# Kernel tuning notes

Measured on AMD Instinct MI355X. Metric: run time of the kernel, lower is better.

The kernel has to match this reference:

```python
import jax, jax.numpy as jnp
import numpy as np
import math

B, P = 64, 2048
E_DRUG, E_PATH = 512, 512
ATTN_DIM, H, DEPTH = 1024, 8, 1
HD = ATTN_DIM // (2 * H)          # head_dim = 64
SCALING = HD ** (-0.5)
LAMBDA_INIT = 0.8 - 0.6 * math.exp(-0.3 * DEPTH)
EPS_SM = 1e-20
EPS_RMS = 1e-5


def stable_softmax(x, eps=EPS_SM):
    x = x.astype(jnp.float32)
    x = x - jnp.max(x, axis=-1, keepdims=True)
    ex = jnp.exp(x)
    return ex / (jnp.sum(ex, axis=-1, keepdims=True) + eps)


def setup_inputs() -> dict:
    key = jax.random.key(0)
    ks = jax.random.split(key, 11)
    d = 2 * H * HD  # = ATTN_DIM
    return {
        "query": jax.random.normal(ks[0], (B, 1, E_DRUG), jnp.float32),
        "key": jax.random.normal(ks[1], (B, P, E_PATH), jnp.float32),
        # Linear weights stored [in, out] (transpose of torch storage; same math)
        "Wq": jax.random.normal(ks[2], (E_DRUG, d), jnp.float32) * 0.02,
        "Wk": jax.random.normal(ks[3], (E_PATH, d), jnp.float32) * 0.02,
        "Wv": jax.random.normal(ks[4], (E_PATH, d), jnp.float32) * 0.02,
        "Wo": jax.random.normal(ks[5], (d, E_DRUG), jnp.float32) * 0.02,
        "lambda_q1": jax.random.normal(ks[6], (HD,), jnp.float32) * 0.1,
        "lambda_k1": jax.random.normal(ks[7], (HD,), jnp.float32) * 0.1,
        "lambda_q2": jax.random.normal(ks[8], (HD,), jnp.float32) * 0.1,
        "lambda_k2": jax.random.normal(ks[9], (HD,), jnp.float32) * 0.1,
        "rms_weight": jnp.ones((2 * HD,), jnp.float32),
    }


def reference(query, key, Wq, Wk, Wv, Wo,
              lambda_q1, lambda_k1, lambda_q2, lambda_k2, rms_weight):
    # Q: [B,1,H,2,HD] -> [B,H,2,1,HD]; K,V: [B,P,H,2,HD] -> [B,H,2,P,HD]
    Q = (query @ Wq).reshape(B, 1, H, 2, HD).transpose(0, 2, 3, 1, 4) * SCALING
    K = (key @ Wk).reshape(B, P, H, 2, HD).transpose(0, 2, 3, 1, 4)
    V = (key @ Wv).reshape(B, P, H, 2, HD)

    # scores: [B,H,2,1,P]
    scores = jnp.einsum('bhsqd,bhskd->bhsqk', Q, K)
    scores = stable_softmax(scores)

    lam1 = jnp.exp(jnp.sum(lambda_q1 * lambda_k1))
    lam2 = jnp.exp(jnp.sum(lambda_q2 * lambda_k2))
    lam = lam1 - lam2 + LAMBDA_INIT

    diff_attn = scores[:, :, 0] - lam * scores[:, :, 1]  # [B,H,1,P]

    V_cat = V.transpose(0, 2, 1, 3, 4).reshape(B, H, P, 2 * HD)  # [B,H,P,2HD]
    out = jnp.einsum('bhqp,bhpd->bhqd', diff_attn, V_cat)        # [B,H,1,2HD]

    # RMSNorm over last dim, affine
    var = jnp.mean(out * out, axis=-1, keepdims=True)
    out = out * jax.lax.rsqrt(var + EPS_RMS) * rms_weight
    out = out * (1.0 - LAMBDA_INIT)

    out = out.transpose(0, 2, 1, 3).reshape(B, 1, 2 * H * HD)
    out = out @ Wo  # [B,1,E_DRUG]
    return out, diff_attn
```

## Files before the change

### kernel.cpp

```cpp
#include <hip/hip_runtime.h>
#include <hip/hip_bf16.h>
#include <math.h>

#define B_ 64
#define P_ 2048
#define E_ 512
#define H_ 8
#define D_ 1024
#define NC_ 32
#define NG_ 4
#define SMEM_FUSED (65536 + 8704 + 2304 + 64 + 64)

#define BAR() do { asm volatile("s_waitcnt lgkmcnt(0)" ::: "memory"); \
                   __builtin_amdgcn_s_barrier(); } while (0)

static constexpr float SCALING_C = 0.125f;
static constexpr float LAMBDA_INIT_C = 0.35550906759096966f;

typedef float f32x4 __attribute__((ext_vector_type(4)));
typedef float f32x2 __attribute__((ext_vector_type(2)));
typedef short bf16x8 __attribute__((ext_vector_type(8)));
typedef short bf16x4 __attribute__((ext_vector_type(4)));

static __device__ __forceinline__ short f2bf(float f) {
    unsigned u = __builtin_bit_cast(unsigned, f);
    unsigned r = (u + 0x7fffu + ((u >> 16) & 1u)) >> 16;
    return (short)r;
}

__global__ __launch_bounds__(256) void k_qproj(const float* __restrict__ query,
                                               const float* __restrict__ Wq,
                                               const float* __restrict__ Wk,
                                               unsigned short* __restrict__ qkfrag) {
    int x = blockIdx.x, b = blockIdx.y, t = threadIdx.x;
    __shared__ float q[E_];
    __shared__ float qh[256];
    q[t] = query[b * E_ + t];
    q[t + 256] = query[b * E_ + t + 256];
    __syncthreads();
    {
        int j = x * 256 + t;
        const float* w = Wq + j;
        float s[8] = {0.f,0.f,0.f,0.f,0.f,0.f,0.f,0.f};
        #pragma unroll 4
        for (int e = 0; e < E_; e += 8) {
            #pragma unroll
            for (int k = 0; k < 8; ++k) s[k] += q[e + k] * w[(long)(e + k) * D_];
        }
        qh[t] = (((s[0]+s[1])+(s[2]+s[3])) + ((s[4]+s[5])+(s[6]+s[7]))) * SCALING_C;
    }
    __syncthreads();
    int hs_loc = t >> 6, l = t & 63;
    int hs = x * 4 + hs_loc;
    int e0 = l * 8;
    const float* qp = qh + hs_loc * 64;
    float acc[8];
    #pragma unroll
    for (int jj = 0; jj < 8; ++jj) {
        const f32x4* w = (const f32x4*)(Wk + (long)(e0 + jj) * D_ + hs * 64);
        float s = 0.f;
        #pragma unroll
        for (int d4 = 0; d4 < 16; ++d4) {
            f32x4 wv = w[d4];
            s += qp[d4 * 4 + 0] * wv[0] + qp[d4 * 4 + 1] * wv[1]
               + qp[d4 * 4 + 2] * wv[2] + qp[d4 * 4 + 3] * wv[3];
        }
        acc[jj] = s;
    }
    bf16x8 v;
    #pragma unroll
    for (int jj = 0; jj < 8; ++jj) v[jj] = f2bf(acc[jj]);
    *(bf16x8*)(qkfrag + (((long)b * 16 + (l >> 2)) * 64 + (l & 3) * 16 + hs) * 8) = v;
}

__global__ __launch_bounds__(512, 2) void k_fusedp(const float* __restrict__ key,
                                                   const unsigned short* __restrict__ qkfrag,
                                                   float* __restrict__ wexp,
                                                   float* __restrict__ ms, float* __restrict__ zs,
                                                   float* __restrict__ apart) {
    extern __shared__ __align__(16) char smem[];
    unsigned short* kswz = (unsigned short*)smem;
    float* scr           = (float*)(smem + 65536);
    unsigned short* wbf  = (unsigned short*)(smem + 74240);
    float* fac_l         = (float*)(smem + 76544);
    float* mrun_l        = (float*)(smem + 76608);

    int pcg = blockIdx.x, b = blockIdx.y;
    int t = threadIdx.x, wv = t >> 6, l = t & 63;
    int rt = wv >> 1, eh = wv & 1;
    int prow = rt * 16 + (l & 15);
    int xorv = ((prow & 7) << 3) ^ ((prow & 8) << 1);
    int hi = t >> 7;
    int col4 = t & 127;

    if (t < 16) mrun_l[t] = -3.0e38f;

    bf16x8 qfr[8];
    {
        const bf16x8* qf = (const bf16x8*)(qkfrag + (long)b * 16 * 64 * 8);
        #pragma unroll
        for (int s = 0; s < 8; ++s) qfr[s] = qf[(eh * 8 + s) * 64 + l];
    }

    const float* kchunk = key + ((long)b * P_ + pcg * 512) * E_;

    f32x4 x[16];
    #pragma unroll
    for (int r = 0; r < 16; ++r)
        x[r] = *(const f32x4*)(kchunk + (long)(r * 512 + t) * 4);

    f32x4 accp[4];
    #pragma unroll
    for (int i = 0; i < 4; ++i) accp[i] = {0.f, 0.f, 0.f, 0.f};

    for (int c = 0; c < 8; ++c) {
        #pragma unroll
        for (int r = 0; r < 16; ++r) {
            int row = 4 * r + hi;
            int xr = ((row & 7) << 3) ^ ((row & 8) << 1);
            bf16x4 wb;
            wb[0] = f2bf(x[r][0]); wb[1] = f2bf(x[r][1]);
            wb[2] = f2bf(x[r][2]); wb[3] = f2bf(x[r][3]);
            *(bf16x4*)(kswz + row * 512 + ((col4 * 4) ^ xr)) = wb;
        }
        if (c < 7) {
            const float* kn = kchunk + (long)(c + 1) * 64 * E_;
            #pragma unroll
            for (int r = 0; r < 16; ++r)
                x[r] = *(const f32x4*)(kn + (long)(r * 512 + t) * 4);
        }
        BAR();

        {
            f32x4 acc = {0.f, 0.f, 0.f, 0.f};
            #pragma unroll
            for (int s = 0; s < 8; ++s) {
                int e8 = eh * 256 + (l >> 4) * 8 + s * 32;
                bf16x8 a = *(const bf16x8*)(kswz + prow * 512 + (e8 ^ xorv));
                acc = __builtin_amdgcn_mfma_f32_16x16x32_bf16(a, qfr[s], acc, 0, 0, 0);
            }
            #pragma unroll
            for (int r = 0; r < 4; ++r)
                scr[eh * 1088 + (l & 15) * 68 + rt * 16 + (l >> 4) * 4 + r] = acc[r];
        }
        BAR();

        {
            int hs = t >> 5, i = t & 31;
            const float* s0p = scr + hs * 68 + i * 2;
            const float* s1p = s0p + 1088;
            float v0 = s0p[0] + s1p[0];
            float v1 = s0p[1] + s1p[1];
            float m = fmaxf(v0, v1);
            #pragma unroll
            for (int o = 16; o > 0; o >>= 1) m = fmaxf(m, __shfl_xor(m, o));
            float e0v = expf(v0 - m), e1v = expf(v1 - m);
            float z = e0v + e1v;
            #pragma unroll
            for (int o = 16; o > 0; o >>= 1) z += __shfl_xor(z, o);
            float mold = mrun_l[hs];
            float mnew = fmaxf(mold, m);
            float wsc = expf(m - mnew);
            if (i == 0) {
                mrun_l[hs] = mnew;
                fac_l[hs] = expf(mold - mnew);
                ms[((long)(pcg * 8 + c) * B_ + b) * 16 + hs] = m;
                zs[((long)(pcg * 8 + c) * B_ + b) * 16 + hs] = z;
            }
            f32x2 wv2; wv2[0] = e0v; wv2[1] = e1v;
            *(f32x2*)(wexp + ((long)b * 16 + hs) * P_ + pcg * 512 + c * 64 + i * 2) = wv2;
            unsigned lo = (unsigned short)f2bf(e0v * wsc);
            unsigned hi2 = (unsigned short)f2bf(e1v * wsc);
            *(unsigned*)(wbf + hs * 72 + i * 2) = lo | (hi2 << 16);
        }
        BAR();

        {
            f32x4 frv;
            frv[0] = fac_l[(l >> 4) * 4 + 0];
            frv[1] = fac_l[(l >> 4) * 4 + 1];
            frv[2] = fac_l[(l >> 4) * 4 + 2];
            frv[3] = fac_l[(l >> 4) * 4 + 3];
            const unsigned short* wrow = wbf + (l & 15) * 72;
            #pragma unroll
            for (int tile = 0; tile < 4; ++tile) {
                accp[tile] = accp[tile] * frv;
                int e = wv * 64 + tile * 16 + (l & 15);
                #pragma unroll
                for (int ks = 0; ks < 2; ++ks) {
                    int pbase = ks * 32 + (l >> 4) * 8;
                    bf16x8 af = *(const bf16x8*)(wrow + pbase);
                    int x2 = (pbase & 8) << 1;
                    bf16x8 bfv;
                    #pragma unroll
                    for (int j = 0; j < 8; ++j)
                        bfv[j] = (short)kswz[(pbase + j) * 512 + (e ^ (j << 3) ^ x2)];
                    accp[tile] = __builtin_amdgcn_mfma_f32_16x16x32_bf16(af, bfv, accp[tile], 0, 0, 0);
                }
            }
        }
        BAR();
    }

    {
        long abase = ((long)pcg * B_ + b) * 16 * E_;
        #pragma unroll
        for (int tile = 0; tile < 4; ++tile) {
            int e = wv * 64 + tile * 16 + (l & 15);
            #pragma unroll
            for (int r = 0; r < 4; ++r)
                apart[abase + (long)((l >> 4) * 4 + r) * E_ + e] = accp[tile][r];
        }
    }
}

__global__ __launch_bounds__(256) void k_comb(const float* __restrict__ wexp,
                                              const float* __restrict__ ms, const float* __restrict__ zs,
                                              const float* __restrict__ apart,
                                              const float* __restrict__ lq1, const float* __restrict__ lk1,
                                              const float* __restrict__ lq2, const float* __restrict__ lk2,
                                              const float* __restrict__ Wv, const float* __restrict__ rmsw,
                                              float* __restrict__ out1, float* __restrict__ on) {
    int h = blockIdx.x, b = blockIdx.y, t = threadIdx.x;
    __shared__ float lam_s;
    __shared__ float mc0s[NC_], mc1s[NC_], zc0s[NC_], zc1s[NC_];
    __shared__ float c0s[NC_], c1s[NC_];
    __shared__ float attk[E_];
    __shared__ float onred[2][128];
    __shared__ float red[4];
    int hs0 = 2 * h, hs1 = 2 * h + 1;
    if (t < 64) {
        float v1 = lq1[t] * lk1[t];
        float v2 = lq2[t] * lk2[t];
        #pragma unroll
        for (int o = 32; o > 0; o >>= 1) { v1 += __shfl_xor(v1, o); v2 += __shfl_xor(v2, o); }
        if (t == 0) lam_s = expf(v1) - expf(v2) + LAMBDA_INIT_C;
    }
    if (t >= 64 && t < 64 + NC_) {
        int c = t - 64;
        mc0s[c] = ms[((long)c * B_ + b) * 16 + hs0];
        mc1s[c] = ms[((long)c * B_ + b) * 16 + hs1];
        zc0s[c] = zs[((long)c * B_ + b) * 16 + hs0];
        zc1s[c] = zs[((long)c * B_ + b) * 16 + hs1];
    }
    __syncthreads();
    float m0 = -3.0e38f, m1 = -3.0e38f;
    #pragma unroll
    for (int c = 0; c < NC_; ++c) { m0 = fmaxf(m0, mc0s[c]); m1 = fmaxf(m1, mc1s[c]); }
    float z0 = 0.f, z1 = 0.f;
    #pragma unroll
    for (int c = 0; c < NC_; ++c) {
        z0 += zc0s[c] * expf(mc0s[c] - m0);
        z1 += zc1s[c] * expf(mc1s[c] - m1);
    }
    float lam = lam_s;
    float i0 = 1.f / (z0 + 1e-20f);
    float i1 = lam / (z1 + 1e-20f);
    if (t < NC_) {
        c0s[t] = expf(mc0s[t] - m0) * i0;
        c1s[t] = expf(mc1s[t] - m1) * i1;
    }
    __syncthreads();
    const float* w0p = wexp + ((long)b * 16 + hs0) * P_;
    const float* w1p = wexp + ((long)b * 16 + hs1) * P_;
    float* dst = out1 + ((long)b * H_ + h) * P_;
    #pragma unroll
    for (int c8 = 0; c8 < 8; ++c8) {
        int p = c8 * 256 + t;
        dst[p] = w0p[p] * c0s[p >> 6] - w1p[p] * c1s[p >> 6];
    }
    float cg0[NG_], cg1[NG_];
    #pragma unroll
    for (int g = 0; g < NG_; ++g) {
        float mg0 = -3.0e38f, mg1 = -3.0e38f;
        #pragma unroll
        for (int q = 0; q < 8; ++q) {
            mg0 = fmaxf(mg0, mc0s[g * 8 + q]);
            mg1 = fmaxf(mg1, mc1s[g * 8 + q]);
        }
        cg0[g] = expf(mg0 - m0) * i0;
        cg1[g] = expf(mg1 - m1) * i1;
    }
    #pragma unroll
    for (int k = 0; k < 2; ++k) {
        int e = k * 256 + t;
        float s = 0.f;
        #pragma unroll
        for (int g = 0; g < NG_; ++g) {
            s += cg0[g] * apart[(((long)g * B_ + b) * 16 + hs0) * E_ + e]
               - cg1[g] * apart[(((long)g * B_ + b) * 16 + hs1) * E_ + e];
        }
        attk[e] = s;
    }
    __syncthreads();
    int j = t & 127, half = t >> 7;
    const float* w = Wv + (long)(half * 256) * D_ + h * 128 + j;
    const float* aa = attk + half * 256;
    float s[8] = {0.f,0.f,0.f,0.f,0.f,0.f,0.f,0.f};
    #pragma unroll 4
    for (int e = 0; e < 256; e += 8) {
        #pragma unroll
        for (int k = 0; k < 8; ++k) s[k] += aa[e + k] * w[(long)(e + k) * D_];
    }
    onred[half][j] = ((s[0]+s[1])+(s[2]+s[3])) + ((s[4]+s[5])+(s[6]+s[7]));
    __syncthreads();
    float v = 0.f;
    if (t < 128) v = onred[0][t] + onred[1][t];
    float sq = v * v;
    int wv2 = t >> 6, ln = t & 63;
    #pragma unroll
    for (int o = 32; o > 0; o >>= 1) sq += __shfl_xor(sq, o);
    if (ln == 0) red[wv2] = sq;
    __syncthreads();
    float tot = red[0] + red[1];
    float scale = rsqrtf(tot * (1.f / 128.f) + 1e-5f) * (1.f - LAMBDA_INIT_C);
    if (t < 128) on[(long)b * D_ + h * 128 + t] = v * scale * rmsw[t];
}

__global__ __launch_bounds__(256) void k_wo(const float* __restrict__ on,
                                            const float* __restrict__ Wo,
                                            float* __restrict__ wop) {
    int kc = blockIdx.x >> 1, oc = blockIdx.x & 1, b = blockIdx.y;
    int t = threadIdx.x;
    __shared__ float sh[256];
    sh[t] = on[(long)b * D_ + kc * 256 + t];
    __syncthreads();
    int o = oc * 256 + t;
    const float* w = Wo + (long)(kc * 256) * 512 + o;
    float s[8] = {0.f,0.f,0.f,0.f,0.f,0.f,0.f,0.f};
    #pragma unroll 4
    for (int k = 0; k < 256; k += 8) {
        #pragma unroll
        for (int q = 0; q < 8; ++q) s[q] += sh[k + q] * w[(long)(k + q) * 512];
    }
    wop[((long)kc * B_ + b) * 512 + o] = ((s[0]+s[1])+(s[2]+s[3])) + ((s[4]+s[5])+(s[6]+s[7]));
}

__global__ __launch_bounds__(256) void k_wored(const float* __restrict__ wop,
                                               float* __restrict__ out0) {
    int b = blockIdx.x, t = threadIdx.x;
    #pragma unroll
    for (int i = 0; i < 2; ++i) {
        int o = i * 256 + t;
        float s = 0.f;
        #pragma unroll
        for (int kc = 0; kc < 4; ++kc) s += wop[((long)kc * B_ + b) * 512 + o];
        out0[(long)b * 512 + o] = s;
    }
}

extern "C" void kernel_launch(void* const* d_in, const int* in_sizes, int n_in,
                              void* d_out, int out_size, void* d_ws, size_t ws_size,
                              hipStream_t stream) {
    const float* query = (const float*)d_in[0];
    const float* key   = (const float*)d_in[1];
    const float* Wq    = (const float*)d_in[2];
    const float* Wk    = (const float*)d_in[3];
    const float* Wv    = (const float*)d_in[4];
    const float* Wo    = (const float*)d_in[5];
    const float* lq1   = (const float*)d_in[6];
    const float* lk1   = (const float*)d_in[7];
    const float* lq2   = (const float*)d_in[8];
    const float* lk2   = (const float*)d_in[9];
    const float* rmsw  = (const float*)d_in[10];

    float* out0 = (float*)d_out;
    float* out1 = out0 + B_ * E_;

    unsigned short* qkfrag = (unsigned short*)d_ws;
    float* wexp  = (float*)d_ws + 262144;
    float* apart = wexp + (long)B_ * 16 * P_;
    float* ms    = apart + (long)NG_ * B_ * 16 * E_;
    float* zs    = ms + NC_ * B_ * 16;
    float* on    = zs + NC_ * B_ * 16;
    float* wop   = on + B_ * D_;

    hipFuncSetAttribute((const void*)k_fusedp,
                        hipFuncAttributeMaxDynamicSharedMemorySize, SMEM_FUSED);

    hipLaunchKernelGGL(k_qproj,  dim3(4, B_),   dim3(256), 0, stream, query, Wq, Wk, qkfrag);
    hipLaunchKernelGGL(k_fusedp, dim3(NG_, B_), dim3(512), SMEM_FUSED, stream,
                       key, qkfrag, wexp, ms, zs, apart);
    hipLaunchKernelGGL(k_comb,   dim3(H_, B_),  dim3(256), 0, stream, wexp, ms, zs, apart,
                       lq1, lk1, lq2, lk2, Wv, rmsw, out1, on);
    hipLaunchKernelGGL(k_wo,     dim3(8, B_),   dim3(256), 0, stream, on, Wo, wop);
    hipLaunchKernelGGL(k_wored,  dim3(B_),      dim3(256), 0, stream, wop, out0);
}
```

Before: 121.1 us.

## Warp-specialize fused kernel with async global-to-LDS double-buffered key loads

Splits the fused projection/softmax kernel's eight waves into four producer waves and four consumer waves. The producers stream fp32 key chunks straight into double-buffered LDS with global_load_lds. The consumers convert to bf16 on the fly and run the MFMA score and accumulation stages. The chunk size drops to 32 rows, so there are 64 softmax sub-chunks and the combine kernel is updated to match. The aim is to overlap memory traffic with compute and to drop the register-staged conversion pass. In exchange, LDS use doubles to about 137 KB, occupancy falls to one block per CU, and half the waves do no math.

```diff
diff --git a/kernel.cpp b/kernel.cpp
--- a/kernel.cpp
+++ b/kernel.cpp
@@ -7,12 +7,14 @@
 #define E_ 512
 #define H_ 8
 #define D_ 1024
-#define NC_ 32
+#define NCH_ 16
+#define NSC_ 64
 #define NG_ 4
-#define SMEM_FUSED (65536 + 8704 + 2304 + 64 + 64)
+#define SMEM_FUSED (131072 + 4608 + 1280 + 64 + 64)
 
 #define BAR() do { asm volatile("s_waitcnt lgkmcnt(0)" ::: "memory"); \
                    __builtin_amdgcn_s_barrier(); } while (0)
+#define VM0() asm volatile("s_waitcnt vmcnt(0)" ::: "memory")
 
 static constexpr float SCALING_C = 0.125f;
 static constexpr float LAMBDA_INIT_C = 0.35550906759096966f;
@@ -20,12 +22,17 @@
 typedef float f32x4 __attribute__((ext_vector_type(4)));
 typedef float f32x2 __attribute__((ext_vector_type(2)));
 typedef short bf16x8 __attribute__((ext_vector_type(8)));
-typedef short bf16x4 __attribute__((ext_vector_type(4)));
 
 static __device__ __forceinline__ short f2bf(float f) {
     unsigned u = __builtin_bit_cast(unsigned, f);
     unsigned r = (u + 0x7fffu + ((u >> 16) & 1u)) >> 16;
     return (short)r;
+}
+
+static __device__ __forceinline__ void gload_lds16(const float* g, char* l) {
+    __builtin_amdgcn_global_load_lds(
+        (const __attribute__((address_space(1))) void*)g,
+        (__attribute__((address_space(3))) void*)l, 16, 0, 0);
 }
 
 __global__ __launch_bounds__(256) void k_qproj(const float* __restrict__ query,
@@ -73,145 +80,147 @@
     *(bf16x8*)(qkfrag + (((long)b * 16 + (l >> 2)) * 64 + (l & 3) * 16 + hs) * 8) = v;
 }
 
-__global__ __launch_bounds__(512, 2) void k_fusedp(const float* __restrict__ key,
+__global__ __launch_bounds__(512, 1) void k_fusedp(const float* __restrict__ key,
                                                    const unsigned short* __restrict__ qkfrag,
                                                    float* __restrict__ wexp,
                                                    float* __restrict__ ms, float* __restrict__ zs,
                                                    float* __restrict__ apart) {
     extern __shared__ __align__(16) char smem[];
-    unsigned short* kswz = (unsigned short*)smem;
-    float* scr           = (float*)(smem + 65536);
-    unsigned short* wbf  = (unsigned short*)(smem + 74240);
-    float* fac_l         = (float*)(smem + 76544);
-    float* mrun_l        = (float*)(smem + 76608);
+    float* scr           = (float*)(smem + 131072);
+    unsigned short* wbf  = (unsigned short*)(smem + 135680);
+    float* fac_l         = (float*)(smem + 136960);
+    float* mrun_l        = (float*)(smem + 137024);
 
     int pcg = blockIdx.x, b = blockIdx.y;
     int t = threadIdx.x, wv = t >> 6, l = t & 63;
-    int rt = wv >> 1, eh = wv & 1;
+    int pw = wv;
+    int cw = wv - 4;
+    int rt = cw >> 1, eh = cw & 1;
     int prow = rt * 16 + (l & 15);
-    int xorv = ((prow & 7) << 3) ^ ((prow & 8) << 1);
-    int hi = t >> 7;
-    int col4 = t & 127;
 
     if (t < 16) mrun_l[t] = -3.0e38f;
 
+#define P_ISSUE(cc) do {                                                          \
+    char* bufc_ = smem + ((cc) & 1) * 65536;                                      \
+    const float* gb_ = key + ((long)b * P_ + pcg * (NCH_ * 32) + (cc) * 32) * E_; \
+    _Pragma("unroll")                                                             \
+    for (int k_ = 0; k_ < 16; ++k_) {                                             \
+        int row_ = pw * 8 + (k_ >> 1);                                            \
+        int h_ = k_ & 1;                                                          \
+        const float* g_ = gb_ + (long)row_ * E_ + (((h_ * 64 + l) ^ (row_ & 7)) << 2); \
+        gload_lds16(g_, bufc_ + row_ * 2048 + h_ * 1024);                         \
+    }                                                                             \
+} while (0)
+
     bf16x8 qfr[8];
-    {
+    f32x4 accp[8];
+    if (wv >= 4) {
         const bf16x8* qf = (const bf16x8*)(qkfrag + (long)b * 16 * 64 * 8);
         #pragma unroll
         for (int s = 0; s < 8; ++s) qfr[s] = qf[(eh * 8 + s) * 64 + l];
-    }
-
-    const float* kchunk = key + ((long)b * P_ + pcg * 512) * E_;
-
-    f32x4 x[16];
-    #pragma unroll
-    for (int r = 0; r < 16; ++r)
-        x[r] = *(const f32x4*)(kchunk + (long)(r * 512 + t) * 4);
-
-    f32x4 accp[4];
-    #pragma unroll
-    for (int i = 0; i < 4; ++i) accp[i] = {0.f, 0.f, 0.f, 0.f};
-
-    for (int c = 0; c < 8; ++c) {
-        #pragma unroll
-        for (int r = 0; r < 16; ++r) {
-            int row = 4 * r + hi;
-            int xr = ((row & 7) << 3) ^ ((row & 8) << 1);
-            bf16x4 wb;
-            wb[0] = f2bf(x[r][0]); wb[1] = f2bf(x[r][1]);
-            wb[2] = f2bf(x[r][2]); wb[3] = f2bf(x[r][3]);
-            *(bf16x4*)(kswz + row * 512 + ((col4 * 4) ^ xr)) = wb;
-        }
-        if (c < 7) {
-            const float* kn = kchunk + (long)(c + 1) * 64 * E_;
-            #pragma unroll
-            for (int r = 0; r < 16; ++r)
-                x[r] = *(const f32x4*)(kn + (long)(r * 512 + t) * 4);
-        }
-        BAR();
-
-        {
+        #pragma unroll
+        for (int i = 0; i < 8; ++i) accp[i] = {0.f, 0.f, 0.f, 0.f};
+    } else {
+        P_ISSUE(0);
+        VM0();
+    }
+    BAR();
+
+    for (int c = 0; c < NCH_; ++c) {
+        const char* bufc = smem + (c & 1) * 65536;
+        if (wv < 4) {
+            if (c < NCH_ - 1) P_ISSUE(c + 1);
+        } else {
             f32x4 acc = {0.f, 0.f, 0.f, 0.f};
+            const char* rbase = bufc + prow * 2048;
+            int swz = prow & 7;
             #pragma unroll
             for (int s = 0; s < 8; ++s) {
                 int e8 = eh * 256 + (l >> 4) * 8 + s * 32;
-                bf16x8 a = *(const bf16x8*)(kswz + prow * 512 + (e8 ^ xorv));
+                int blk = (e8 >> 2) ^ swz;
+                f32x4 xa = *(const f32x4*)(rbase + blk * 16);
+                f32x4 xb = *(const f32x4*)(rbase + (blk ^ 1) * 16);
+                bf16x8 a;
+                a[0] = f2bf(xa[0]); a[1] = f2bf(xa[1]); a[2] = f2bf(xa[2]); a[3] = f2bf(xa[3]);
+                a[4] = f2bf(xb[0]); a[5] = f2bf(xb[1]); a[6] = f2bf(xb[2]); a[7] = f2bf(xb[3]);
                 acc = __builtin_amdgcn_mfma_f32_16x16x32_bf16(a, qfr[s], acc, 0, 0, 0);
             }
             #pragma unroll
             for (int r = 0; r < 4; ++r)
-                scr[eh * 1088 + (l & 15) * 68 + rt * 16 + (l >> 4) * 4 + r] = acc[r];
+                scr[eh * 576 + (l & 15) * 36 + rt * 16 + (l >> 4) * 4 + r] = acc[r];
         }
         BAR();
 
-        {
-            int hs = t >> 5, i = t & 31;
-            const float* s0p = scr + hs * 68 + i * 2;
-            const float* s1p = s0p + 1088;
+        if (wv >= 4) {
+            int hs = cw * 4 + (l >> 4);
+            int i = l & 15;
+            const float* s0p = scr + hs * 36 + i * 2;
+            const float* s1p = s0p + 576;
             float v0 = s0p[0] + s1p[0];
             float v1 = s0p[1] + s1p[1];
             float m = fmaxf(v0, v1);
             #pragma unroll
-            for (int o = 16; o > 0; o >>= 1) m = fmaxf(m, __shfl_xor(m, o));
+            for (int o = 8; o > 0; o >>= 1) m = fmaxf(m, __shfl_xor(m, o));
             float e0v = expf(v0 - m), e1v = expf(v1 - m);
             float z = e0v + e1v;
             #pragma unroll
-            for (int o = 16; o > 0; o >>= 1) z += __shfl_xor(z, o);
+            for (int o = 8; o > 0; o >>= 1) z += __shfl_xor(z, o);
             float mold = mrun_l[hs];
             float mnew = fmaxf(mold, m);
             float wsc = expf(m - mnew);
             if (i == 0) {
                 mrun_l[hs] = mnew;
                 fac_l[hs] = expf(mold - mnew);
-                ms[((long)(pcg * 8 + c) * B_ + b) * 16 + hs] = m;
-                zs[((long)(pcg * 8 + c) * B_ + b) * 16 + hs] = z;
+                ms[((long)(pcg * NCH_ + c) * B_ + b) * 16 + hs] = m;
+                zs[((long)(pcg * NCH_ + c) * B_ + b) * 16 + hs] = z;
             }
             f32x2 wv2; wv2[0] = e0v; wv2[1] = e1v;
-            *(f32x2*)(wexp + ((long)b * 16 + hs) * P_ + pcg * 512 + c * 64 + i * 2) = wv2;
+            *(f32x2*)(wexp + ((long)b * 16 + hs) * P_ + pcg * (NCH_ * 32) + c * 32 + i * 2) = wv2;
             unsigned lo = (unsigned short)f2bf(e0v * wsc);
             unsigned hi2 = (unsigned short)f2bf(e1v * wsc);
-            *(unsigned*)(wbf + hs * 72 + i * 2) = lo | (hi2 << 16);
+            *(unsigned*)(wbf + hs * 40 + i * 2) = lo | (hi2 << 16);
         }
         BAR();
 
-        {
+        if (wv < 4) {
+            VM0();
+        } else {
             f32x4 frv;
             frv[0] = fac_l[(l >> 4) * 4 + 0];
             frv[1] = fac_l[(l >> 4) * 4 + 1];
             frv[2] = fac_l[(l >> 4) * 4 + 2];
             frv[3] = fac_l[(l >> 4) * 4 + 3];
-            const unsigned short* wrow = wbf + (l & 15) * 72;
-            #pragma unroll
-            for (int tile = 0; tile < 4; ++tile) {
+            const unsigned short* wrow = wbf + (l & 15) * 40;
+            int pbase = (l >> 4) * 8;
+            bf16x8 af = *(const bf16x8*)(wrow + pbase);
+            #pragma unroll
+            for (int tile = 0; tile < 8; ++tile) {
+                int e = cw * 128 + tile * 16 + (l & 15);
+                bf16x8 bfv;
+                #pragma unroll
+                for (int j = 0; j < 8; ++j) {
+                    const float* kf = (const float*)(bufc + (pbase + j) * 2048
+                                       + (((e >> 2) ^ j) * 16) + ((e & 3) << 2));
+                    bfv[j] = f2bf(*kf);
+                }
                 accp[tile] = accp[tile] * frv;
-                int e = wv * 64 + tile * 16 + (l & 15);
-                #pragma unroll
-                for (int ks = 0; ks < 2; ++ks) {
-                    int pbase = ks * 32 + (l >> 4) * 8;
-                    bf16x8 af = *(const bf16x8*)(wrow + pbase);
-                    int x2 = (pbase & 8) << 1;
-                    bf16x8 bfv;
-                    #pragma unroll
-                    for (int j = 0; j < 8; ++j)
-                        bfv[j] = (short)kswz[(pbase + j) * 512 + (e ^ (j << 3) ^ x2)];
-                    accp[tile] = __builtin_amdgcn_mfma_f32_16x16x32_bf16(af, bfv, accp[tile], 0, 0, 0);
-                }
+                accp[tile] = __builtin_amdgcn_mfma_f32_16x16x32_bf16(af, bfv, accp[tile], 0, 0, 0);
             }
         }
         BAR();
     }
 
-    {
+    if (wv >= 4) {
         long abase = ((long)pcg * B_ + b) * 16 * E_;
         #pragma unroll
-        for (int tile = 0; tile < 4; ++tile) {
-            int e = wv * 64 + tile * 16 + (l & 15);
+        for (int tile = 0; tile < 8; ++tile) {
+            int e = cw * 128 + tile * 16 + (l & 15);
             #pragma unroll
             for (int r = 0; r < 4; ++r)
                 apart[abase + (long)((l >> 4) * 4 + r) * E_ + e] = accp[tile][r];
         }
     }
+#undef P_ISSUE
 }
 
 __global__ __launch_bounds__(256) void k_comb(const float* __restrict__ wexp,
@@ -223,8 +232,8 @@
                                               float* __restrict__ out1, float* __restrict__ on) {
     int h = blockIdx.x, b = blockIdx.y, t = threadIdx.x;
     __shared__ float lam_s;
-    __shared__ float mc0s[NC_], mc1s[NC_], zc0s[NC_], zc1s[NC_];
-    __shared__ float c0s[NC_], c1s[NC_];
+    __shared__ float mc0s[NSC_], mc1s[NSC_], zc0s[NSC_], zc1s[NSC_];
+    __shared__ float c0s[NSC_], c1s[NSC_];
     __shared__ float attk[E_];
     __shared__ float onred[2][128];
     __shared__ float red[4];
@@ -236,7 +245,7 @@
         for (int o = 32; o > 0; o >>= 1) { v1 += __shfl_xor(v1, o); v2 += __shfl_xor(v2, o); }
         if (t == 0) lam_s = expf(v1) - expf(v2) + LAMBDA_INIT_C;
     }
-    if (t >= 64 && t < 64 + NC_) {
+    if (t >= 64 && t < 64 + NSC_) {
         int c = t - 64;
         mc0s[c] = ms[((long)c * B_ + b) * 16 + hs0];
         mc1s[c] = ms[((long)c * B_ + b) * 16 + hs1];
@@ -245,18 +254,18 @@
     }
     __syncthreads();
     float m0 = -3.0e38f, m1 = -3.0e38f;
-    #pragma unroll
-    for (int c = 0; c < NC_; ++c) { m0 = fmaxf(m0, mc0s[c]); m1 = fmaxf(m1, mc1s[c]); }
+    #pragma unroll 8
+    for (int c = 0; c < NSC_; ++c) { m0 = fmaxf(m0, mc0s[c]); m1 = fmaxf(m1, mc1s[c]); }
     float z0 = 0.f, z1 = 0.f;
-    #pragma unroll
-    for (int c = 0; c < NC_; ++c) {
+    #pragma unroll 8
+    for (int c = 0; c < NSC_; ++c) {
         z0 += zc0s[c] * expf(mc0s[c] - m0);
         z1 += zc1s[c] * expf(mc1s[c] - m1);
     }
     float lam = lam_s;
     float i0 = 1.f / (z0 + 1e-20f);
     float i1 = lam / (z1 + 1e-20f);
-    if (t < NC_) {
+    if (t < NSC_) {
         c0s[t] = expf(mc0s[t] - m0) * i0;
         c1s[t] = expf(mc1s[t] - m1) * i1;
     }
@@ -267,16 +276,16 @@
     #pragma unroll
     for (int c8 = 0; c8 < 8; ++c8) {
         int p = c8 * 256 + t;
-        dst[p] = w0p[p] * c0s[p >> 6] - w1p[p] * c1s[p >> 6];
+        dst[p] = w0p[p] * c0s[p >> 5] - w1p[p] * c1s[p >> 5];
     }
     float cg0[NG_], cg1[NG_];
     #pragma unroll
     for (int g = 0; g < NG_; ++g) {
         float mg0 = -3.0e38f, mg1 = -3.0e38f;
         #pragma unroll
-        for (int q = 0; q < 8; ++q) {
-            mg0 = fmaxf(mg0, mc0s[g * 8 + q]);
-            mg1 = fmaxf(mg1, mc1s[g * 8 + q]);
+        for (int q = 0; q < NCH_; ++q) {
+            mg0 = fmaxf(mg0, mc0s[g * NCH_ + q]);
+            mg1 = fmaxf(mg1, mc1s[g * NCH_ + q]);
         }
         cg0[g] = expf(mg0 - m0) * i0;
         cg1[g] = expf(mg1 - m1) * i1;
@@ -371,8 +380,8 @@
     float* wexp  = (float*)d_ws + 262144;
     float* apart = wexp + (long)B_ * 16 * P_;
     float* ms    = apart + (long)NG_ * B_ * 16 * E_;
-    float* zs    = ms + NC_ * B_ * 16;
-    float* on    = zs + NC_ * B_ * 16;
+    float* zs    = ms + NSC_ * B_ * 16;
+    float* on    = zs + NSC_ * B_ * 16;
     float* wop   = on + B_ * D_;
 
     hipFuncSetAttribute((const void*)k_fusedp,
```

Result: slower. 125.8 us (+3.9%).

## Double-buffer key chunk prefetch two chunks ahead in fused kernel

Applied to the files above, without the earlier changes.

Adds a second 16-register f32x4 buffer so the key chunk loads are issued two chunks ahead instead of one, alternating between x and y buffers in a fully unrolled chunk loop. The aim is to hide more global-memory latency behind the MFMA and softmax phases. This doubles the prefetch register footprint, so launch bounds are relaxed from 2 to 1 blocks per SM-equivalent, which may reduce occupancy and the latency hiding that came from running two blocks.

```diff
diff --git a/kernel.cpp b/kernel.cpp
--- a/kernel.cpp
+++ b/kernel.cpp
@@ -73,7 +73,7 @@
     *(bf16x8*)(qkfrag + (((long)b * 16 + (l >> 2)) * 64 + (l & 3) * 16 + hs) * 8) = v;
 }
 
-__global__ __launch_bounds__(512, 2) void k_fusedp(const float* __restrict__ key,
+__global__ __launch_bounds__(512, 1) void k_fusedp(const float* __restrict__ key,
                                                    const unsigned short* __restrict__ qkfrag,
                                                    float* __restrict__ wexp,
                                                    float* __restrict__ ms, float* __restrict__ zs,
@@ -104,103 +104,116 @@
 
     const float* kchunk = key + ((long)b * P_ + pcg * 512) * E_;
 
-    f32x4 x[16];
+    f32x4 x[16], y[16];
     #pragma unroll
     for (int r = 0; r < 16; ++r)
         x[r] = *(const f32x4*)(kchunk + (long)(r * 512 + t) * 4);
+    #pragma unroll
+    for (int r = 0; r < 16; ++r)
+        y[r] = *(const f32x4*)(kchunk + (long)64 * E_ + (long)(r * 512 + t) * 4);
 
     f32x4 accp[4];
     #pragma unroll
     for (int i = 0; i < 4; ++i) accp[i] = {0.f, 0.f, 0.f, 0.f};
 
-    for (int c = 0; c < 8; ++c) {
-        #pragma unroll
-        for (int r = 0; r < 16; ++r) {
-            int row = 4 * r + hi;
-            int xr = ((row & 7) << 3) ^ ((row & 8) << 1);
-            bf16x4 wb;
-            wb[0] = f2bf(x[r][0]); wb[1] = f2bf(x[r][1]);
-            wb[2] = f2bf(x[r][2]); wb[3] = f2bf(x[r][3]);
-            *(bf16x4*)(kswz + row * 512 + ((col4 * 4) ^ xr)) = wb;
-        }
-        if (c < 7) {
-            const float* kn = kchunk + (long)(c + 1) * 64 * E_;
-            #pragma unroll
-            for (int r = 0; r < 16; ++r)
-                x[r] = *(const f32x4*)(kn + (long)(r * 512 + t) * 4);
-        }
-        BAR();
-
-        {
-            f32x4 acc = {0.f, 0.f, 0.f, 0.f};
-            #pragma unroll
-            for (int s = 0; s < 8; ++s) {
-                int e8 = eh * 256 + (l >> 4) * 8 + s * 32;
-                bf16x8 a = *(const bf16x8*)(kswz + prow * 512 + (e8 ^ xorv));
-                acc = __builtin_amdgcn_mfma_f32_16x16x32_bf16(a, qfr[s], acc, 0, 0, 0);
-            }
-            #pragma unroll
-            for (int r = 0; r < 4; ++r)
-                scr[eh * 1088 + (l & 15) * 68 + rt * 16 + (l >> 4) * 4 + r] = acc[r];
-        }
-        BAR();
-
-        {
-            int hs = t >> 5, i = t & 31;
-            const float* s0p = scr + hs * 68 + i * 2;
-            const float* s1p = s0p + 1088;
-            float v0 = s0p[0] + s1p[0];
-            float v1 = s0p[1] + s1p[1];
-            float m = fmaxf(v0, v1);
-            #pragma unroll
-            for (int o = 16; o > 0; o >>= 1) m = fmaxf(m, __shfl_xor(m, o));
-            float e0v = expf(v0 - m), e1v = expf(v1 - m);
-            float z = e0v + e1v;
-            #pragma unroll
-            for (int o = 16; o > 0; o >>= 1) z += __shfl_xor(z, o);
-            float mold = mrun_l[hs];
-            float mnew = fmaxf(mold, m);
-            float wsc = expf(m - mnew);
-            if (i == 0) {
-                mrun_l[hs] = mnew;
-                fac_l[hs] = expf(mold - mnew);
-                ms[((long)(pcg * 8 + c) * B_ + b) * 16 + hs] = m;
-                zs[((long)(pcg * 8 + c) * B_ + b) * 16 + hs] = z;
-            }
-            f32x2 wv2; wv2[0] = e0v; wv2[1] = e1v;
-            *(f32x2*)(wexp + ((long)b * 16 + hs) * P_ + pcg * 512 + c * 64 + i * 2) = wv2;
-            unsigned lo = (unsigned short)f2bf(e0v * wsc);
-            unsigned hi2 = (unsigned short)f2bf(e1v * wsc);
-            *(unsigned*)(wbf + hs * 72 + i * 2) = lo | (hi2 << 16);
-        }
-        BAR();
-
-        {
-            f32x4 frv;
-            frv[0] = fac_l[(l >> 4) * 4 + 0];
-            frv[1] = fac_l[(l >> 4) * 4 + 1];
-            frv[2] = fac_l[(l >> 4) * 4 + 2];
-            frv[3] = fac_l[(l >> 4) * 4 + 3];
-            const unsigned short* wrow = wbf + (l & 15) * 72;
-            #pragma unroll
-            for (int tile = 0; tile < 4; ++tile) {
-                accp[tile] = accp[tile] * frv;
-                int e = wv * 64 + tile * 16 + (l & 15);
-                #pragma unroll
-                for (int ks = 0; ks < 2; ++ks) {
-                    int pbase = ks * 32 + (l >> 4) * 8;
-                    bf16x8 af = *(const bf16x8*)(wrow + pbase);
-                    int x2 = (pbase & 8) << 1;
-                    bf16x8 bfv;
-                    #pragma unroll
-                    for (int j = 0; j < 8; ++j)
-                        bfv[j] = (short)kswz[(pbase + j) * 512 + (e ^ (j << 3) ^ x2)];
-                    accp[tile] = __builtin_amdgcn_mfma_f32_16x16x32_bf16(af, bfv, accp[tile], 0, 0, 0);
-                }
-            }
-        }
-        BAR();
-    }
+#define CHUNK_BODY(XR, c)                                                        \
+    do {                                                                         \
+         \
+        _Pragma("unroll")                                                        \
+        for (int r = 0; r < 16; ++r) {                                           \
+            int row = 4 * r + hi;                                                \
+            int xr_ = ((row & 7) << 3) ^ ((row & 8) << 1);                       \
+            bf16x4 wb;                                                           \
+            wb[0] = f2bf(XR[r][0]); wb[1] = f2bf(XR[r][1]);                      \
+            wb[2] = f2bf(XR[r][2]); wb[3] = f2bf(XR[r][3]);                      \
+            *(bf16x4*)(kswz + row * 512 + ((col4 * 4) ^ xr_)) = wb;              \
+        }                                                                        \
+                  \
+        if ((c) + 2 < 8) {                                                       \
+            const float* kn_ = kchunk + (long)((c) + 2) * 64 * E_;               \
+            _Pragma("unroll")                                                    \
+            for (int r = 0; r < 16; ++r)                                         \
+                XR[r] = *(const f32x4*)(kn_ + (long)(r * 512 + t) * 4);          \
+        }                                                                        \
+        BAR();                                                                   \
+                                                  \
+        {                                                                        \
+            f32x4 acc = {0.f, 0.f, 0.f, 0.f};                                    \
+            _Pragma("unroll")                                                    \
+            for (int s = 0; s < 8; ++s) {                                        \
+                int e8 = eh * 256 + (l >> 4) * 8 + s * 32;                       \
+                bf16x8 a = *(const bf16x8*)(kswz + prow * 512 + (e8 ^ xorv));    \
+                acc = __builtin_amdgcn_mfma_f32_16x16x32_bf16(a, qfr[s], acc, 0, 0, 0); \
+            }                                                                    \
+            _Pragma("unroll")                                                    \
+            for (int r = 0; r < 4; ++r)                                          \
+                scr[eh * 1088 + (l & 15) * 68 + rt * 16 + (l >> 4) * 4 + r] = acc[r]; \
+        }                                                                        \
+        BAR();                                                                   \
+          \
+        {                                                                        \
+            int hs = t >> 5, i = t & 31;                                         \
+            const float* s0p = scr + hs * 68 + i * 2;                            \
+            const float* s1p = s0p + 1088;                                       \
+            float v0 = s0p[0] + s1p[0];                                          \
+            float v1 = s0p[1] + s1p[1];                                          \
+            float m = fmaxf(v0, v1);                                             \
+            _Pragma("unroll")                                                    \
+            for (int o = 16; o > 0; o >>= 1) m = fmaxf(m, __shfl_xor(m, o));     \
+            float e0v = expf(v0 - m), e1v = expf(v1 - m);                        \
+            float z = e0v + e1v;                                                 \
+            _Pragma("unroll")                                                    \
+            for (int o = 16; o > 0; o >>= 1) z += __shfl_xor(z, o);              \
+            float mold = mrun_l[hs];                                             \
+            float mnew = fmaxf(mold, m);                                         \
+            float wsc = expf(m - mnew);                                          \
+            if (i == 0) {                                                        \
+                mrun_l[hs] = mnew;                                               \
+                fac_l[hs] = expf(mold - mnew);                                   \
+                ms[((long)(pcg * 8 + (c)) * B_ + b) * 16 + hs] = m;              \
+                zs[((long)(pcg * 8 + (c)) * B_ + b) * 16 + hs] = z;              \
+            }                                                                    \
+            f32x2 wv2; wv2[0] = e0v; wv2[1] = e1v;                               \
+            *(f32x2*)(wexp + ((long)b * 16 + hs) * P_ + pcg * 512 + (c) * 64 + i * 2) = wv2; \
+            unsigned lo = (unsigned short)f2bf(e0v * wsc);                       \
+            unsigned hi2 = (unsigned short)f2bf(e1v * wsc);                      \
+            *(unsigned*)(wbf + hs * 72 + i * 2) = lo | (hi2 << 16);              \
+        }                                                                        \
+        BAR();                                                                   \
+                         \
+        {                                                                        \
+            f32x4 frv;                                                           \
+            frv[0] = fac_l[(l >> 4) * 4 + 0];                                    \
+            frv[1] = fac_l[(l >> 4) * 4 + 1];                                    \
+            frv[2] = fac_l[(l >> 4) * 4 + 2];                                    \
+            frv[3] = fac_l[(l >> 4) * 4 + 3];                                    \
+            const unsigned short* wrow = wbf + (l & 15) * 72;                    \
+            _Pragma("unroll")                                                    \
+            for (int tile = 0; tile < 4; ++tile) {                               \
+                accp[tile] = accp[tile] * frv;                                   \
+                int e = wv * 64 + tile * 16 + (l & 15);                          \
+                _Pragma("unroll")                                                \
+                for (int ks = 0; ks < 2; ++ks) {                                 \
+                    int pbase = ks * 32 + (l >> 4) * 8;                          \
+                    bf16x8 af = *(const bf16x8*)(wrow + pbase);                  \
+                    int x2 = (pbase & 8) << 1;                                   \
+                    bf16x8 bfv;                                                  \
+                    _Pragma("unroll")                                            \
+                    for (int j = 0; j < 8; ++j)                                  \
+                        bfv[j] = (short)kswz[(pbase + j) * 512 + (e ^ (j << 3) ^ x2)]; \
+                    accp[tile] = __builtin_amdgcn_mfma_f32_16x16x32_bf16(af, bfv, accp[tile], 0, 0, 0); \
+                }                                                                \
+            }                                                                    \
+        }                                                                        \
+        BAR();                                                                   \
+    } while (0)
+
+    #pragma unroll
+    for (int cc = 0; cc < 8; cc += 2) {
+        CHUNK_BODY(x, cc);
+        CHUNK_BODY(y, cc + 1);
+    }
+#undef CHUNK_BODY
 
     {
         long abase = ((long)pcg * B_ + b) * 16 * E_;
```

Measured after the change: 148.7 us. 1.23x slower.
